# Kernel tuning notes

Hardware: AMD Instinct MI355X
Metric: run time of the kernel (lower is better)

Reference implementation:

```python
import jax, jax.numpy as jnp
import numpy as np

M_TOKENS, D_IN, D_OUT = 4096, 4096, 16384


def setup_inputs() -> dict:
    key = jax.random.key(0)
    k1, k2, k3, k4 = jax.random.split(key, 4)
    x = jax.random.normal(k1, (M_TOKENS, D_IN), dtype=jnp.float32)
    # pre-quantized int8 weight, stored [K, N] as in qweight_kn
    qweight_kn = jax.random.randint(k2, (D_IN, D_OUT), -127, 128, dtype=jnp.int8)
    # per-output-channel weight dequant scales (float16 buffer, used as fp32 in kernel)
    weight_scales = jax.random.uniform(k3, (D_OUT,), dtype=jnp.float32, minval=1e-3, maxval=2e-2)
    bias = jax.random.normal(k4, (D_OUT,), dtype=jnp.float32) * 0.01
    return {"x": x, "qweight_kn": qweight_kn, "weight_scales": weight_scales, "bias": bias}


def reference(x, qweight_kn, weight_scales, bias):
    target_dtype = x.dtype
    x2 = x.reshape(-1, x.shape[-1])  # [M, K]
    # dynamic per-token (per-row) symmetric quantization
    x_max = jnp.max(jnp.abs(x2), axis=-1, keepdims=True).astype(jnp.float32) + 1e-5
    x_scales = x_max / 127.0  # [M, 1]
    x_int8 = jnp.clip(jnp.round(x2.astype(jnp.float32) / x_scales), -128, 127).astype(jnp.int8)
    acc = jax.lax.dot_general(
        x_int8, qweight_kn,
        dimension_numbers=(((1,), (0,)), ((), ())),
        preferred_element_type=jnp.int32,
    )  # [M, N] int32
    # fused dequant: row act-scale * col weight-scale, plus bias
    c = acc.astype(jnp.float32) * x_scales * weight_scales[None, :].astype(jnp.float32)
    c = c + bias[None, :]
    out = c.astype(jnp.bfloat16)  # kernel stores bf16
    return out.reshape(*x.shape[:-1], -1).astype(target_dtype)
```

## Files before the change

### kernel.cpp

```cpp
#include <hip/hip_runtime.h>
#include <hip/hip_bf16.h>
#include <stdint.h>

typedef int v4i __attribute__((ext_vector_type(4)));

#define GM 4096
#define GN 16384
#define GK 4096
#define BM 256
#define BN 256
#define BK 128
#define NTILES (GK / BK)

__device__ __forceinline__ void gload16(const void* g, void* l) {
  __builtin_amdgcn_global_load_lds(
      (const __attribute__((address_space(1))) void*)g,
      (__attribute__((address_space(3))) void*)l, 16, 0, 0);
}

__global__ __launch_bounds__(256) void quant_rows(
    const float* __restrict__ x, int8_t* __restrict__ xq,
    float* __restrict__ xs, int K) {
  const int row = blockIdx.x;
  const int t = threadIdx.x;
  const float4* src = (const float4*)(x + (size_t)row * K) + t * 4;
  float4 v[4];
  float m = 0.f;
#pragma unroll
  for (int i = 0; i < 4; ++i) {
    v[i] = src[i];
    m = fmaxf(m, fmaxf(fmaxf(fabsf(v[i].x), fabsf(v[i].y)),
                       fmaxf(fabsf(v[i].z), fabsf(v[i].w))));
  }
#pragma unroll
  for (int off = 1; off < 64; off <<= 1)
    m = fmaxf(m, __shfl_xor(m, off, 64));
  __shared__ float wmax[4];
  if ((t & 63) == 0) wmax[t >> 6] = m;
  __syncthreads();
  const float gm = fmaxf(fmaxf(wmax[0], wmax[1]), fmaxf(wmax[2], wmax[3]));
  const float scale = (gm + 1e-5f) / 127.0f;
  if (t == 0) xs[row] = scale;
  unsigned packed[4];
#pragma unroll
  for (int i = 0; i < 4; ++i) {
    float fv[4] = {v[i].x, v[i].y, v[i].z, v[i].w};
    unsigned p = 0;
#pragma unroll
    for (int j = 0; j < 4; ++j) {
      int q = (int)rintf(fv[j] / scale);
      q = max(-128, min(127, q));
      p |= (unsigned)(q & 0xff) << (8 * j);
    }
    packed[i] = p;
  }
  *(int4*)(xq + (size_t)row * K + t * 16) =
      make_int4((int)packed[0], (int)packed[1], (int)packed[2], (int)packed[3]);
}

__global__ __launch_bounds__(256) void transpose_pack(
    const int* __restrict__ W32, int8_t* __restrict__ Wt, int K, int N) {
  __shared__ __align__(16) int8_t tile[64][80];
  const int t = threadIdx.x;
  const int n0 = blockIdx.x * 64;
  const int k0 = blockIdx.y * 64;
  const int ln = t & 63;
  const int wv = t >> 6;
#pragma unroll
  for (int it = 0; it < 16; ++it) {
    const int kk = wv * 16 + it;
    tile[ln][kk] = (int8_t)W32[(size_t)(k0 + kk) * N + n0 + ln];
  }
  __syncthreads();
  const int kb = wv * 16;
  const int4 v = *(const int4*)&tile[ln][kb];
  *(int4*)(Wt + (size_t)(n0 + ln) * K + k0 + kb) = v;
}

__global__ __launch_bounds__(512, 2) void gemm_i8(
    const int8_t* __restrict__ Xq, const int8_t* __restrict__ Wt,
    const float* __restrict__ xs, const float* __restrict__ wsc,
    const float* __restrict__ bias, float* __restrict__ C) {
  __shared__ __align__(16) int8_t lA[2][BM][BK];
  __shared__ __align__(16) int8_t lB[2][BN][BK];

  const int t = threadIdx.x;
  const int lane = t & 63;
  const int w = t >> 6;
  const int wr = w >> 2;
  const int wc = w & 3;
  const int fr = lane & 15;
  const int kg = lane >> 4;

  const int bid = blockIdx.x;
  const int xcd = bid & 7;
  const int q = bid >> 3;
  const int tm = q & 15;
  const int tn = xcd * 8 + (q >> 4);
  const size_t rowA0 = (size_t)tm * BM;
  const size_t rowB0 = (size_t)tn * BN;

  const int8_t* XqB = Xq + rowA0 * GK;
  const int8_t* WtB = Wt + rowB0 * GK;
  int srcOff[4], dstOff[4];
#pragma unroll
  for (int i = 0; i < 4; ++i) {
    const int slot0 = (i * 8 + w) * 64;
    const int slot = slot0 + lane;
    const int r = slot >> 3;
    const int c = (slot & 7) ^ (r & 7);
    srcOff[i] = r * GK + c * 16;
    dstOff[i] = slot0 * 16;
  }

#define STAGE(KT, D)                                                       \
  {                                                                        \
    const int ko = (KT)*BK;                                                \
    _Pragma("unroll") for (int i = 0; i < 4; ++i)                          \
        gload16(XqB + srcOff[i] + ko, (int8_t*)&lA[(D)][0][0] + dstOff[i]);\
    _Pragma("unroll") for (int i = 0; i < 4; ++i)                          \
        gload16(WtB + srcOff[i] + ko, (int8_t*)&lB[(D)][0][0] + dstOff[i]);\
  }

  const int ck0 = (((0 * 4) + kg) ^ (fr & 7)) * 16;
  const int ck1 = (((1 * 4) + kg) ^ (fr & 7)) * 16;

#define LDA_ROW(DSTI, MI, D)                                        \
  {                                                                 \
    const int8_t* p = &lA[(D)][wr * 128 + (MI)*16 + fr][0];         \
    areg[DSTI][0] = *(const v4i*)(p + ck0);                         \
    areg[DSTI][1] = *(const v4i*)(p + ck1);                         \
  }
#define LDB_ROW(NJ, D)                                              \
  {                                                                 \
    const int8_t* p = &lB[(D)][wc * 64 + (NJ)*16 + fr][0];          \
    breg[NJ][0] = *(const v4i*)(p + ck0);                           \
    breg[NJ][1] = *(const v4i*)(p + ck1);                           \
  }

#define MFMA_QUAD(MI0, NJ0)                                                    \
  _Pragma("unroll") for (int mi = 0; mi < 4; ++mi)                             \
      _Pragma("unroll") for (int nj = 0; nj < 2; ++nj) {                       \
    acc[(MI0) + mi][(NJ0) + nj] = __builtin_amdgcn_mfma_i32_16x16x64_i8(       \
        areg[mi][0], breg[(NJ0) + nj][0], acc[(MI0) + mi][(NJ0) + nj], 0, 0, 0);\
    acc[(MI0) + mi][(NJ0) + nj] = __builtin_amdgcn_mfma_i32_16x16x64_i8(       \
        areg[mi][1], breg[(NJ0) + nj][1], acc[(MI0) + mi][(NJ0) + nj], 0, 0, 0);\
  }

#define PHASE_TAIL(MI0, NJ0)                                 \
  __builtin_amdgcn_s_barrier();                              \
  asm volatile("s_waitcnt lgkmcnt(0)" ::: "memory");         \
  __builtin_amdgcn_sched_barrier(0);                         \
  __builtin_amdgcn_s_setprio(1);                             \
  MFMA_QUAD(MI0, NJ0);                                       \
  __builtin_amdgcn_s_setprio(0);                             \
  __builtin_amdgcn_s_barrier();

  STAGE(0, 0);
  STAGE(1, 1);
  asm volatile("s_waitcnt vmcnt(8)" ::: "memory");
  __builtin_amdgcn_s_barrier();

  v4i acc[8][4] = {};
  v4i areg[4][2], breg[4][2];

  for (int kt = 0; kt < NTILES; ++kt) {
    const int d = kt & 1;
#pragma unroll
    for (int mi = 0; mi < 4; ++mi) LDA_ROW(mi, mi, d);
    LDB_ROW(0, d);
    LDB_ROW(1, d);
    PHASE_TAIL(0, 0);
    LDB_ROW(2, d);
    LDB_ROW(3, d);
    PHASE_TAIL(0, 2);
#pragma unroll
    for (int mi = 0; mi < 4; ++mi) LDA_ROW(mi, mi + 4, d);
    PHASE_TAIL(4, 0);
    if (kt + 2 < NTILES) STAGE(kt + 2, d);
    __builtin_amdgcn_s_barrier();
    __builtin_amdgcn_s_setprio(1);
    MFMA_QUAD(4, 2);
    __builtin_amdgcn_s_setprio(0);
    if (kt + 2 < NTILES) {
      asm volatile("s_waitcnt vmcnt(8)" ::: "memory");
    } else {
      asm volatile("s_waitcnt vmcnt(0)" ::: "memory");
    }
    __builtin_amdgcn_s_barrier();
  }

  float xsv[8][4];
#pragma unroll
  for (int mi = 0; mi < 8; ++mi)
#pragma unroll
    for (int r = 0; r < 4; ++r)
      xsv[mi][r] = xs[rowA0 + wr * 128 + mi * 16 + kg * 4 + r];
#pragma unroll
  for (int nj = 0; nj < 4; ++nj) {
    const int col_l = wc * 64 + nj * 16 + fr;
    const float wsv = wsc[rowB0 + col_l];
    const float bv = bias[rowB0 + col_l];
#pragma unroll
    for (int mi = 0; mi < 8; ++mi) {
#pragma unroll
      for (int r = 0; r < 4; ++r) {
        const size_t row = rowA0 + wr * 128 + mi * 16 + kg * 4 + r;
        const float f = (float)acc[mi][nj][r] * xsv[mi][r] * wsv + bv;
        C[row * GN + rowB0 + col_l] = __bfloat162float(__float2bfloat16(f));
      }
    }
  }
}

extern "C" void kernel_launch(void* const* d_in, const int* in_sizes, int n_in,
                              void* d_out, int out_size, void* d_ws, size_t ws_size,
                              hipStream_t stream) {
  const int M = GM, K = GK, N = GN;
  const float* x = (const float*)d_in[0];
  const int* W32 = (const int*)d_in[1];
  const float* wsc = (const float*)d_in[2];
  const float* bias = (const float*)d_in[3];
  float* out = (float*)d_out;

  float* xs = (float*)d_ws;
  int8_t* Xq = (int8_t*)d_ws + 16384;
  int8_t* Wt = (int8_t*)d_ws + 16384 + (size_t)M * K;

  transpose_pack<<<dim3(N / 64, K / 64), 256, 0, stream>>>(W32, Wt, K, N);
  quant_rows<<<M, 256, 0, stream>>>(x, Xq, xs, K);
  gemm_i8<<<dim3((M / BM) * (N / BN)), 512, 0, stream>>>(Xq, Wt, xs, wsc, bias,
                                                         out);
}
```

Baseline: 494.3 us.

## Restructure int8 GEMM main loop to prefetch LDS fragments and cut barriers

The per-tile loop is reordered so all B fragments and the upper A fragments are issued up front, with graded lgkmcnt waits gating each MFMA group, and the next tile's lower A fragments are prefetched before the last MFMA block. The number of workgroup barriers per K-tile drops from seven to two. LDS reads and MFMA work should overlap more and less time is spent synchronizing. In exchange it uses more registers for the extra A fragment set, which risks spills or lower occupancy. The next global stage is also issued later in the iteration.

```diff
diff --git a/kernel.cpp b/kernel.cpp
--- a/kernel.cpp
+++ b/kernel.cpp
@@ -113,81 +113,88 @@
     dstOff[i] = slot0 * 16;
   }
 
-#define STAGE(KT, D)                                                       \
-  {                                                                        \
-    const int ko = (KT)*BK;                                                \
-    _Pragma("unroll") for (int i = 0; i < 4; ++i)                          \
-        gload16(XqB + srcOff[i] + ko, (int8_t*)&lA[(D)][0][0] + dstOff[i]);\
-    _Pragma("unroll") for (int i = 0; i < 4; ++i)                          \
-        gload16(WtB + srcOff[i] + ko, (int8_t*)&lB[(D)][0][0] + dstOff[i]);\
-  }
-
-  const int ck0 = (((0 * 4) + kg) ^ (fr & 7)) * 16;
-  const int ck1 = (((1 * 4) + kg) ^ (fr & 7)) * 16;
-
-#define LDA_ROW(DSTI, MI, D)                                        \
-  {                                                                 \
-    const int8_t* p = &lA[(D)][wr * 128 + (MI)*16 + fr][0];         \
-    areg[DSTI][0] = *(const v4i*)(p + ck0);                         \
-    areg[DSTI][1] = *(const v4i*)(p + ck1);                         \
-  }
-#define LDB_ROW(NJ, D)                                              \
-  {                                                                 \
-    const int8_t* p = &lB[(D)][wc * 64 + (NJ)*16 + fr][0];          \
-    breg[NJ][0] = *(const v4i*)(p + ck0);                           \
-    breg[NJ][1] = *(const v4i*)(p + ck1);                           \
-  }
-
-#define MFMA_QUAD(MI0, NJ0)                                                    \
-  _Pragma("unroll") for (int mi = 0; mi < 4; ++mi)                             \
-      _Pragma("unroll") for (int nj = 0; nj < 2; ++nj) {                       \
-    acc[(MI0) + mi][(NJ0) + nj] = __builtin_amdgcn_mfma_i32_16x16x64_i8(       \
-        areg[mi][0], breg[(NJ0) + nj][0], acc[(MI0) + mi][(NJ0) + nj], 0, 0, 0);\
-    acc[(MI0) + mi][(NJ0) + nj] = __builtin_amdgcn_mfma_i32_16x16x64_i8(       \
-        areg[mi][1], breg[(NJ0) + nj][1], acc[(MI0) + mi][(NJ0) + nj], 0, 0, 0);\
-  }
-
-#define PHASE_TAIL(MI0, NJ0)                                 \
-  __builtin_amdgcn_s_barrier();                              \
-  asm volatile("s_waitcnt lgkmcnt(0)" ::: "memory");         \
-  __builtin_amdgcn_sched_barrier(0);                         \
-  __builtin_amdgcn_s_setprio(1);                             \
-  MFMA_QUAD(MI0, NJ0);                                       \
-  __builtin_amdgcn_s_setprio(0);                             \
-  __builtin_amdgcn_s_barrier();
+#define STAGE(KT, D)                                                        \
+  {                                                                         \
+    const int ko = (KT)*BK;                                                 \
+    _Pragma("unroll") for (int i = 0; i < 4; ++i)                           \
+        gload16(XqB + srcOff[i] + ko, (int8_t*)&lA[(D)][0][0] + dstOff[i]); \
+    _Pragma("unroll") for (int i = 0; i < 4; ++i)                           \
+        gload16(WtB + srcOff[i] + ko, (int8_t*)&lB[(D)][0][0] + dstOff[i]); \
+  }
+
+  const int ck0 = ((0 + kg) ^ (fr & 7)) * 16;
+  const int ck1 = ((4 + kg) ^ (fr & 7)) * 16;
+
+  v4i acc[8][4] = {};
+  v4i areg[4][2], aregh[4][2], breg[4][2];
+
+#define ISSUE_A_LO(D)                                                \
+  _Pragma("unroll") for (int mi = 0; mi < 4; ++mi) {                 \
+    const int8_t* p = &lA[(D)][wr * 128 + mi * 16 + fr][0];          \
+    areg[mi][0] = *(const v4i*)(p + ck0);                            \
+    areg[mi][1] = *(const v4i*)(p + ck1);                            \
+  }
+#define ISSUE_A_HI(D)                                                \
+  _Pragma("unroll") for (int mi = 0; mi < 4; ++mi) {                 \
+    const int8_t* p = &lA[(D)][wr * 128 + 64 + mi * 16 + fr][0];     \
+    aregh[mi][0] = *(const v4i*)(p + ck0);                           \
+    aregh[mi][1] = *(const v4i*)(p + ck1);                           \
+  }
+#define ISSUE_B(NJ, D)                                               \
+  {                                                                  \
+    const int8_t* p = &lB[(D)][wc * 64 + (NJ)*16 + fr][0];           \
+    breg[NJ][0] = *(const v4i*)(p + ck0);                            \
+    breg[NJ][1] = *(const v4i*)(p + ck1);                            \
+  }
+
+#define MFMA_Q(AR, MI0, NJ0)                                                    \
+  _Pragma("unroll") for (int mi = 0; mi < 4; ++mi)                              \
+      _Pragma("unroll") for (int nj = 0; nj < 2; ++nj) {                        \
+    acc[(MI0) + mi][(NJ0) + nj] = __builtin_amdgcn_mfma_i32_16x16x64_i8(        \
+        AR[mi][0], breg[(NJ0) + nj][0], acc[(MI0) + mi][(NJ0) + nj], 0, 0, 0);  \
+    acc[(MI0) + mi][(NJ0) + nj] = __builtin_amdgcn_mfma_i32_16x16x64_i8(        \
+        AR[mi][1], breg[(NJ0) + nj][1], acc[(MI0) + mi][(NJ0) + nj], 0, 0, 0);  \
+  }
 
   STAGE(0, 0);
   STAGE(1, 1);
   asm volatile("s_waitcnt vmcnt(8)" ::: "memory");
   __builtin_amdgcn_s_barrier();
-
-  v4i acc[8][4] = {};
-  v4i areg[4][2], breg[4][2];
+  ISSUE_A_LO(0);
 
   for (int kt = 0; kt < NTILES; ++kt) {
     const int d = kt & 1;
-#pragma unroll
-    for (int mi = 0; mi < 4; ++mi) LDA_ROW(mi, mi, d);
-    LDB_ROW(0, d);
-    LDB_ROW(1, d);
-    PHASE_TAIL(0, 0);
-    LDB_ROW(2, d);
-    LDB_ROW(3, d);
-    PHASE_TAIL(0, 2);
-#pragma unroll
-    for (int mi = 0; mi < 4; ++mi) LDA_ROW(mi, mi + 4, d);
-    PHASE_TAIL(4, 0);
-    if (kt + 2 < NTILES) STAGE(kt + 2, d);
+    ISSUE_B(0, d);
+    ISSUE_B(1, d);
+    ISSUE_B(2, d);
+    ISSUE_B(3, d);
+    ISSUE_A_HI(d);
+    asm volatile("s_waitcnt lgkmcnt(12)" ::: "memory");
+    __builtin_amdgcn_sched_barrier(0);
+    __builtin_amdgcn_s_setprio(1);
+    MFMA_Q(areg, 0, 0);
+    __builtin_amdgcn_s_setprio(0);
+    asm volatile("s_waitcnt lgkmcnt(8)" ::: "memory");
+    __builtin_amdgcn_sched_barrier(0);
+    __builtin_amdgcn_s_setprio(1);
+    MFMA_Q(areg, 0, 2);
+    __builtin_amdgcn_s_setprio(0);
+    asm volatile("s_waitcnt lgkmcnt(0)" ::: "memory");
+    __builtin_amdgcn_sched_barrier(0);
     __builtin_amdgcn_s_barrier();
-    __builtin_amdgcn_s_setprio(1);
-    MFMA_QUAD(4, 2);
-    __builtin_amdgcn_s_setprio(0);
     if (kt + 2 < NTILES) {
+      STAGE(kt + 2, d);
       asm volatile("s_waitcnt vmcnt(8)" ::: "memory");
     } else {
       asm volatile("s_waitcnt vmcnt(0)" ::: "memory");
     }
     __builtin_amdgcn_s_barrier();
+    if (kt + 1 < NTILES) { ISSUE_A_LO(d ^ 1); }
+    __builtin_amdgcn_sched_barrier(0);
+    __builtin_amdgcn_s_setprio(1);
+    MFMA_Q(aregh, 4, 0);
+    MFMA_Q(aregh, 4, 2);
+    __builtin_amdgcn_s_setprio(0);
   }
 
   float xsv[8][4];
```

Result: slower. 506.9 us (+2.5%).

## Switch GEMM to 4-slot BK=64 LDS ring with one barrier per tile

Applied to the files above, without the earlier changes.

Halves the K-tile to 64 and uses a four-deep LDS ring buffer with prefetch distance three, replacing the double-buffered BK=128 loop. Each tile now needs a single barrier instead of several, and finer lgkmcnt waits let MFMAs start as soon as their fragments arrive. The aim is to cut synchronisation stalls and keep more global loads in flight. In exchange the loop runs twice as many iterations. The ring also issues wrapped, unneeded loads for the last three tiles, and the epilogue now reads xs per element instead of caching it in registers.

```diff
diff --git a/kernel.cpp b/kernel.cpp
--- a/kernel.cpp
+++ b/kernel.cpp
@@ -9,8 +9,9 @@
 #define GK 4096
 #define BM 256
 #define BN 256
-#define BK 128
-#define NTILES (GK / BK)
+#define BK 64
+#define NT (GK / BK)
+#define SLOT_BYTES 16384
 
 __device__ __forceinline__ void gload16(const void* g, void* l) {
   __builtin_amdgcn_global_load_lds(
@@ -81,8 +82,8 @@
     const int8_t* __restrict__ Xq, const int8_t* __restrict__ Wt,
     const float* __restrict__ xs, const float* __restrict__ wsc,
     const float* __restrict__ bias, float* __restrict__ C) {
-  __shared__ __align__(16) int8_t lA[2][BM][BK];
-  __shared__ __align__(16) int8_t lB[2][BN][BK];
+  __shared__ __align__(16) int8_t lA[4][BM * BK];
+  __shared__ __align__(16) int8_t lB[4][BN * BK];
 
   const int t = threadIdx.x;
   const int lane = t & 63;
@@ -102,100 +103,89 @@
 
   const int8_t* XqB = Xq + rowA0 * GK;
   const int8_t* WtB = Wt + rowB0 * GK;
-  int srcOff[4], dstOff[4];
-#pragma unroll
-  for (int i = 0; i < 4; ++i) {
-    const int slot0 = (i * 8 + w) * 64;
+  int srcOff[2], dstOff[2];
+#pragma unroll
+  for (int i = 0; i < 2; ++i) {
+    const int slot0 = (w * 2 + i) * 64;
     const int slot = slot0 + lane;
-    const int r = slot >> 3;
-    const int c = (slot & 7) ^ (r & 7);
+    const int r = slot >> 2;
+    const int c = (slot & 3) ^ (r & 3);
     srcOff[i] = r * GK + c * 16;
     dstOff[i] = slot0 * 16;
   }
 
-#define STAGE(KT, D)                                                       \
-  {                                                                        \
-    const int ko = (KT)*BK;                                                \
-    _Pragma("unroll") for (int i = 0; i < 4; ++i)                          \
-        gload16(XqB + srcOff[i] + ko, (int8_t*)&lA[(D)][0][0] + dstOff[i]);\
-    _Pragma("unroll") for (int i = 0; i < 4; ++i)                          \
-        gload16(WtB + srcOff[i] + ko, (int8_t*)&lB[(D)][0][0] + dstOff[i]);\
-  }
-
-  const int ck0 = (((0 * 4) + kg) ^ (fr & 7)) * 16;
-  const int ck1 = (((1 * 4) + kg) ^ (fr & 7)) * 16;
-
-#define LDA_ROW(DSTI, MI, D)                                        \
-  {                                                                 \
-    const int8_t* p = &lA[(D)][wr * 128 + (MI)*16 + fr][0];         \
-    areg[DSTI][0] = *(const v4i*)(p + ck0);                         \
-    areg[DSTI][1] = *(const v4i*)(p + ck1);                         \
-  }
-#define LDB_ROW(NJ, D)                                              \
-  {                                                                 \
-    const int8_t* p = &lB[(D)][wc * 64 + (NJ)*16 + fr][0];          \
-    breg[NJ][0] = *(const v4i*)(p + ck0);                           \
-    breg[NJ][1] = *(const v4i*)(p + ck1);                           \
-  }
-
-#define MFMA_QUAD(MI0, NJ0)                                                    \
-  _Pragma("unroll") for (int mi = 0; mi < 4; ++mi)                             \
-      _Pragma("unroll") for (int nj = 0; nj < 2; ++nj) {                       \
-    acc[(MI0) + mi][(NJ0) + nj] = __builtin_amdgcn_mfma_i32_16x16x64_i8(       \
-        areg[mi][0], breg[(NJ0) + nj][0], acc[(MI0) + mi][(NJ0) + nj], 0, 0, 0);\
-    acc[(MI0) + mi][(NJ0) + nj] = __builtin_amdgcn_mfma_i32_16x16x64_i8(       \
-        areg[mi][1], breg[(NJ0) + nj][1], acc[(MI0) + mi][(NJ0) + nj], 0, 0, 0);\
-  }
-
-#define PHASE_TAIL(MI0, NJ0)                                 \
-  __builtin_amdgcn_s_barrier();                              \
-  asm volatile("s_waitcnt lgkmcnt(0)" ::: "memory");         \
-  __builtin_amdgcn_sched_barrier(0);                         \
-  __builtin_amdgcn_s_setprio(1);                             \
-  MFMA_QUAD(MI0, NJ0);                                       \
-  __builtin_amdgcn_s_setprio(0);                             \
-  __builtin_amdgcn_s_barrier();
+#define STAGE(KT, SLOT)                                                     \
+  {                                                                         \
+    const int ko = (KT)*BK;                                                 \
+    _Pragma("unroll") for (int i = 0; i < 2; ++i)                           \
+        gload16(XqB + srcOff[i] + ko, &lA[(SLOT)][0] + dstOff[i]);          \
+    _Pragma("unroll") for (int i = 0; i < 2; ++i)                           \
+        gload16(WtB + srcOff[i] + ko, &lB[(SLOT)][0] + dstOff[i]);          \
+  }
+
+  const int ckk = (kg ^ (fr & 3)) * 16;
+
+  v4i acc[8][4] = {};
+  v4i areg[8], breg[4];
+
+#define RD_A(MI, SLOT)                                                      \
+  areg[MI] = *(const v4i*)&lA[(SLOT)][(wr * 128 + (MI)*16 + fr) * BK + ckk];
+#define RD_B(NJ, SLOT)                                                      \
+  breg[NJ] = *(const v4i*)&lB[(SLOT)][(wc * 64 + (NJ)*16 + fr) * BK + ckk];
+
+#define SB __builtin_amdgcn_sched_barrier(0)
+
+#define BODY(T, SLOT)                                                        \
+  {                                                                         \
+     \
+    asm volatile("s_waitcnt vmcnt(8)" ::: "memory");                        \
+    __builtin_amdgcn_s_barrier();                                           \
+    STAGE(((T) + 3) & (NT - 1), ((SLOT) + 3) & 3);                          \
+    SB;                                                                     \
+    RD_A(0, SLOT); RD_A(1, SLOT); RD_A(2, SLOT); RD_A(3, SLOT);             \
+    RD_B(0, SLOT); RD_B(1, SLOT);                                           \
+    SB;                                                                     \
+    RD_B(2, SLOT); RD_B(3, SLOT);                                           \
+    SB;                                                                     \
+    RD_A(4, SLOT); RD_A(5, SLOT); RD_A(6, SLOT); RD_A(7, SLOT);             \
+    SB;                                                                     \
+    asm volatile("s_waitcnt lgkmcnt(6)" ::: "memory");      \
+    SB;                                                                     \
+    __builtin_amdgcn_s_setprio(1);                                          \
+    _Pragma("unroll") for (int mi = 0; mi < 4; ++mi)                        \
+        _Pragma("unroll") for (int nj = 0; nj < 2; ++nj)                    \
+            acc[mi][nj] = __builtin_amdgcn_mfma_i32_16x16x64_i8(            \
+                areg[mi], breg[nj], acc[mi][nj], 0, 0, 0);                  \
+    __builtin_amdgcn_s_setprio(0);                                          \
+    asm volatile("s_waitcnt lgkmcnt(4)" ::: "memory");          \
+    SB;                                                                     \
+    __builtin_amdgcn_s_setprio(1);                                          \
+    _Pragma("unroll") for (int mi = 0; mi < 4; ++mi)                        \
+        _Pragma("unroll") for (int nj = 2; nj < 4; ++nj)                    \
+            acc[mi][nj] = __builtin_amdgcn_mfma_i32_16x16x64_i8(            \
+                areg[mi], breg[nj], acc[mi][nj], 0, 0, 0);                  \
+    __builtin_amdgcn_s_setprio(0);                                          \
+    asm volatile("s_waitcnt lgkmcnt(0)" ::: "memory");           \
+    SB;                                                                     \
+    __builtin_amdgcn_s_setprio(1);                                          \
+    _Pragma("unroll") for (int mi = 4; mi < 8; ++mi)                        \
+        _Pragma("unroll") for (int nj = 0; nj < 4; ++nj)                    \
+            acc[mi][nj] = __builtin_amdgcn_mfma_i32_16x16x64_i8(            \
+                areg[mi], breg[nj], acc[mi][nj], 0, 0, 0);                  \
+    __builtin_amdgcn_s_setprio(0);                                          \
+  }
 
   STAGE(0, 0);
   STAGE(1, 1);
-  asm volatile("s_waitcnt vmcnt(8)" ::: "memory");
-  __builtin_amdgcn_s_barrier();
-
-  v4i acc[8][4] = {};
-  v4i areg[4][2], breg[4][2];
-
-  for (int kt = 0; kt < NTILES; ++kt) {
-    const int d = kt & 1;
-#pragma unroll
-    for (int mi = 0; mi < 4; ++mi) LDA_ROW(mi, mi, d);
-    LDB_ROW(0, d);
-    LDB_ROW(1, d);
-    PHASE_TAIL(0, 0);
-    LDB_ROW(2, d);
-    LDB_ROW(3, d);
-    PHASE_TAIL(0, 2);
-#pragma unroll
-    for (int mi = 0; mi < 4; ++mi) LDA_ROW(mi, mi + 4, d);
-    PHASE_TAIL(4, 0);
-    if (kt + 2 < NTILES) STAGE(kt + 2, d);
-    __builtin_amdgcn_s_barrier();
-    __builtin_amdgcn_s_setprio(1);
-    MFMA_QUAD(4, 2);
-    __builtin_amdgcn_s_setprio(0);
-    if (kt + 2 < NTILES) {
-      asm volatile("s_waitcnt vmcnt(8)" ::: "memory");
-    } else {
-      asm volatile("s_waitcnt vmcnt(0)" ::: "memory");
-    }
-    __builtin_amdgcn_s_barrier();
-  }
-
-  float xsv[8][4];
-#pragma unroll
-  for (int mi = 0; mi < 8; ++mi)
-#pragma unroll
-    for (int r = 0; r < 4; ++r)
-      xsv[mi][r] = xs[rowA0 + wr * 128 + mi * 16 + kg * 4 + r];
+  STAGE(2, 2);
+
+  for (int kt = 0; kt < NT; kt += 4) {
+    BODY(kt, 0);
+    BODY(kt + 1, 1);
+    BODY(kt + 2, 2);
+    BODY(kt + 3, 3);
+  }
+
 #pragma unroll
   for (int nj = 0; nj < 4; ++nj) {
     const int col_l = wc * 64 + nj * 16 + fr;
@@ -206,7 +196,7 @@
 #pragma unroll
       for (int r = 0; r < 4; ++r) {
         const size_t row = rowA0 + wr * 128 + mi * 16 + kg * 4 + r;
-        const float f = (float)acc[mi][nj][r] * xsv[mi][r] * wsv + bv;
+        const float f = (float)acc[mi][nj][r] * xs[row] * wsv + bv;
         C[row * GN + rowB0 + col_l] = __bfloat162float(__float2bfloat16(f));
       }
     }
```

Measured after the change: 503.4 us. No clear change (+1.8%).
